# Kernel tuning notes

Hardware: AMD Instinct MI355X
Metric: run time of the kernel (lower is better)

## Reference

```python
import jax, jax.numpy as jnp
import numpy as np

D_MODEL = 1024
N_HEAD = 16
D_K = D_MODEL // N_HEAD


def setup_inputs() -> dict:
    key = jax.random.key(0)
    ks = jax.random.split(key, 11)
    B, S = 2, 2048
    std = 1.0 / np.sqrt(D_MODEL)
    inp = {
        "Q": jax.random.normal(ks[0], (B, S, D_MODEL), jnp.float32),
        "K": jax.random.normal(ks[1], (B, S, D_MODEL), jnp.float32),
        "V": jax.random.normal(ks[2], (B, S, D_MODEL), jnp.float32),
        "Wq": jax.random.normal(ks[3], (D_MODEL, D_MODEL), jnp.float32) * std,
        "bq": jnp.zeros((D_MODEL,), jnp.float32),
        "Wk": jax.random.normal(ks[4], (D_MODEL, D_MODEL), jnp.float32) * std,
        "bk": jnp.zeros((D_MODEL,), jnp.float32),
        "Wv": jax.random.normal(ks[5], (D_MODEL, D_MODEL), jnp.float32) * std,
        "bv": jnp.zeros((D_MODEL,), jnp.float32),
        "Wo": jax.random.normal(ks[6], (D_MODEL, D_MODEL), jnp.float32) * std,
        "bo": jnp.zeros((D_MODEL,), jnp.float32),
    }
    return inp


def _split_heads(x):
    # [B, S, D] -> [B, H, S, d_k]
    B, S, _ = x.shape
    return x.reshape(B, S, N_HEAD, D_K).transpose(0, 2, 1, 3)


def reference(Q, K, V, Wq, bq, Wk, bk, Wv, bv, Wo, bo):
    q = _split_heads(Q @ Wq.T + bq)   # [B,H,S,dk]
    k = _split_heads(K @ Wk.T + bk)
    v = _split_heads(V @ Wv.T + bv)
    scale = 1.0 / jnp.sqrt(jnp.float32(D_K))
    scores = jnp.einsum("bhqd,bhkd->bhqk", q, k) * scale
    attn = jax.nn.softmax(scores, axis=-1)
    ctx = jnp.einsum("bhqk,bhkd->bhqd", attn, v)  # [B,H,S,dk]
    B, H, S, dk = ctx.shape
    ctx = ctx.transpose(0, 2, 1, 3).reshape(B, S, H * dk)
    return ctx @ Wo.T + bo
```

## Files before the change

kernel.cpp:

```cpp
#include <hip/hip_runtime.h>
#include <hip/hip_bf16.h>
#include <cstdint>
#include <cstddef>
#include <cmath>

typedef __attribute__((ext_vector_type(8))) short short8;
typedef __attribute__((ext_vector_type(4))) short short4_t;
typedef __attribute__((ext_vector_type(4))) float f32x4;
typedef __attribute__((ext_vector_type(16))) float f32x16;

constexpr int B_ = 2, S_ = 2048, H_ = 16, DK_ = 64, DM_ = 1024;

__device__ inline unsigned short f2bf(float x) {
  union { float f; unsigned u; } c; c.f = x;
  unsigned r = c.u + 0x7FFF + ((c.u >> 16) & 1);
  return (unsigned short)(r >> 16);
}

__device__ inline float ex2(float x) {
#if __has_builtin(__builtin_amdgcn_exp2f)
  return __builtin_amdgcn_exp2f(x);
#else
  return exp2f(x);
#endif
}

__device__ inline unsigned pkbf(float lo, float hi) {
  unsigned u;
  asm("v_cvt_pk_bf16_f32 %0, %1, %2" : "=v"(u) : "v"(lo), "v"(hi));
  return u;
}

__device__ inline f32x4 mfma16(short8 a, short8 b, f32x4 c) {
  return __builtin_amdgcn_mfma_f32_16x16x32_bf16(a, b, c, 0, 0, 0);
}
__device__ inline f32x16 mfma32(short8 a, short8 b, f32x16 c) {
  return __builtin_amdgcn_mfma_f32_32x32x16_bf16(a, b, c, 0, 0, 0);
}

__device__ inline void glds16(const unsigned short* g, unsigned short* l) {
  __builtin_amdgcn_global_load_lds(
      (const __attribute__((address_space(1))) unsigned int*)g,
      (__attribute__((address_space(3))) unsigned int*)l, 16, 0, 0);
}

__global__ __launch_bounds__(256) void cvt_all(
    const float* __restrict__ Q, const float* __restrict__ K,
    const float* __restrict__ V, const float* __restrict__ Wq,
    const float* __restrict__ Wk, const float* __restrict__ Wv,
    const float* __restrict__ Wo, unsigned short* __restrict__ Qb,
    unsigned short* __restrict__ Kb, unsigned short* __restrict__ Vb,
    unsigned short* __restrict__ Wqb, unsigned short* __restrict__ Wkb,
    unsigned short* __restrict__ Wvb, unsigned short* __restrict__ Wob) {
  int bid = blockIdx.x;
  const float* in; unsigned short* out; int off;
  if (bid < 4096)       { in = Q;  out = Qb;  off = bid; }
  else if (bid < 8192)  { in = K;  out = Kb;  off = bid - 4096; }
  else if (bid < 12288) { in = V;  out = Vb;  off = bid - 8192; }
  else if (bid < 13312) { in = Wq; out = Wqb; off = bid - 12288; }
  else if (bid < 14336) { in = Wk; out = Wkb; off = bid - 13312; }
  else if (bid < 15360) { in = Wv; out = Wvb; off = bid - 14336; }
  else                  { in = Wo; out = Wob; off = bid - 15360; }
  int i = off * 256 + threadIdx.x;
  float4 f = ((const float4*)in)[i];
  uint2 o;
  o.x = pkbf(f.x, f.y);
  o.y = pkbf(f.z, f.w);
  ((uint2*)out)[i] = o;
}

__device__ inline void store_out(float* p, float v) { *p = v; }
__device__ inline void store_out(unsigned short* p, float v) { *p = f2bf(v); }

template <typename OUT_T>
__device__ inline void gemm_body(const unsigned short* __restrict__ A,
                                 const unsigned short* __restrict__ Bw,
                                 const float* __restrict__ bias,
                                 OUT_T* __restrict__ C, float cscale,
                                 int bm, int bn) {
  constexpr int Kd = 1024, Nd = 1024;
  __shared__ unsigned short As[128][64];
  __shared__ unsigned short Bs[64][64];

  const int tid = threadIdx.x;
  const int lane = tid & 63, wave = tid >> 6;
  const int li = lane & 15, lg = lane >> 4;
  const int wm = wave >> 1, wn = wave & 1;

  const f32x4 zero4 = {0.f, 0.f, 0.f, 0.f};
  f32x4 acc[4][2];
#pragma unroll
  for (int i = 0; i < 4; i++)
#pragma unroll
    for (int j = 0; j < 2; j++) acc[i][j] = zero4;

  const int stg_row = tid >> 3;
  const int stg_col = (tid & 7) * 8;
  const unsigned short* Ag = A + (size_t)(bm * 128 + stg_row) * Kd + stg_col;
  const unsigned short* Bg = Bw + (size_t)(bn * 64 + stg_row) * Kd + stg_col;

  for (int kt = 0; kt < Kd; kt += 64) {
#pragma unroll
    for (int i = 0; i < 4; i++)
      glds16(Ag + (size_t)(i * 32) * Kd + kt, &As[i * 32 + stg_row][stg_col]);
#pragma unroll
    for (int i = 0; i < 2; i++)
      glds16(Bg + (size_t)(i * 32) * Kd + kt, &Bs[i * 32 + stg_row][stg_col]);
    __syncthreads();

    short8 af[4][2], bf[2][2];
#pragma unroll
    for (int kb = 0; kb < 2; kb++) {
#pragma unroll
      for (int i = 0; i < 4; i++)
        af[i][kb] = *(const short8*)&As[wm * 64 + i * 16 + li][kb * 32 + lg * 8];
#pragma unroll
      for (int j = 0; j < 2; j++)
        bf[j][kb] = *(const short8*)&Bs[wn * 32 + j * 16 + li][kb * 32 + lg * 8];
    }
#pragma unroll
    for (int kb = 0; kb < 2; kb++)
#pragma unroll
      for (int i = 0; i < 4; i++)
#pragma unroll
        for (int j = 0; j < 2; j++)
          acc[i][j] = mfma16(af[i][kb], bf[j][kb], acc[i][j]);
    __syncthreads();
  }

#pragma unroll
  for (int j = 0; j < 2; j++) {
    int col = bn * 64 + wn * 32 + j * 16 + li;
    float bv = bias[col];
#pragma unroll
    for (int i = 0; i < 4; i++) {
      int row0 = bm * 128 + wm * 64 + i * 16 + lg * 4;
#pragma unroll
      for (int r = 0; r < 4; r++)
        store_out(&C[(size_t)(row0 + r) * Nd + col], (acc[i][j][r] + bv) * cscale);
    }
  }
}

__global__ __launch_bounds__(256) void gemm_qkv(
    const unsigned short* __restrict__ Aq, const unsigned short* __restrict__ Ak,
    const unsigned short* __restrict__ Av, const unsigned short* __restrict__ Bq,
    const unsigned short* __restrict__ Bk, const unsigned short* __restrict__ Bv,
    const float* __restrict__ bq, const float* __restrict__ bk,
    const float* __restrict__ bv, unsigned short* __restrict__ Cq,
    unsigned short* __restrict__ Ck, unsigned short* __restrict__ Cv,
    float qscale) {
  const int n = blockIdx.x;
  const int xcd = n & 7, m = n >> 3;
  const int z = m >> 6, idx = m & 63;
  const int bm = xcd * 4 + (idx >> 4), bn = idx & 15;
  const unsigned short* A = z == 0 ? Aq : z == 1 ? Ak : Av;
  const unsigned short* Bw = z == 0 ? Bq : z == 1 ? Bk : Bv;
  const float* bi = z == 0 ? bq : z == 1 ? bk : bv;
  unsigned short* C = z == 0 ? Cq : z == 1 ? Ck : Cv;
  gemm_body(A, Bw, bi, C, z == 0 ? qscale : 1.0f, bm, bn);
}

__global__ __launch_bounds__(256) void gemm_out(
    const unsigned short* __restrict__ A, const unsigned short* __restrict__ Bw,
    const float* __restrict__ bias, float* __restrict__ C) {
  const int n = blockIdx.x;
  const int xcd = n & 7, m = n >> 3;
  const int bm = xcd * 4 + (m >> 4), bn = m & 15;
  gemm_body(A, Bw, bias, C, 1.0f, bm, bn);
}

struct V4 { short8 v[4]; };

__device__ __forceinline__ void attn_tile_step(
    int kt, int buf, int NT,
    const unsigned short* kg, const unsigned short* vg,
    unsigned short* KsAll, unsigned short* VtAll,
    int srow, int sc, int scs, int key2, int dq,
    const short8* qf, int l31, int h,
    V4& vc, V4& vn, f32x16* po, float& m_i, float& l_i) {
  unsigned short* KsB = KsAll + buf * (128 * 64);
  unsigned short* VtB = VtAll + buf * (64 * 128);
  unsigned short* KsO = KsAll + (buf ^ 1) * (128 * 64);

  asm volatile("s_waitcnt vmcnt(0)" ::: "memory");
  __builtin_amdgcn_sched_barrier(0);

#pragma unroll
  for (int j = 0; j < 16; j++) {
    const int half = j >> 3, jj = j & 7;
    unsigned w = (unsigned)(unsigned short)vc.v[half][jj] |
                 ((unsigned)(unsigned short)vc.v[2 + half][jj] << 16);
    const int slot = (key2 >> 3) ^ j;
    *(unsigned*)&VtB[(dq * 16 + j) * 128 + slot * 8 + (key2 & 7)] = w;
  }

  if (kt + 1 < NT) {
    const unsigned short* vp =
        vg + (size_t)((kt + 1) * 128 + key2) * DM_ + dq * 16;
    vn.v[0] = *(const short8*)(vp);
    vn.v[1] = *(const short8*)(vp + 8);
    vn.v[2] = *(const short8*)(vp + DM_);
    vn.v[3] = *(const short8*)(vp + DM_ + 8);
  }

  asm volatile("s_waitcnt lgkmcnt(0)" ::: "memory");
  __builtin_amdgcn_sched_barrier(0);
  __builtin_amdgcn_s_barrier();
  __builtin_amdgcn_sched_barrier(0);

  if (kt + 1 < NT) {
    const unsigned short* kgt = kg + (size_t)((kt + 1) * 128) * DM_;
#pragma unroll
    for (int i = 0; i < 4; i++)
      glds16(kgt + (size_t)(i * 32 + srow) * DM_ + scs,
             &KsO[(i * 32 + srow) * 64 + sc * 8]);
  }
  __builtin_amdgcn_sched_barrier(0);

  f32x16 sacc[4];
#pragma unroll
  for (int kb = 0; kb < 4; kb++)
#pragma unroll
    for (int r = 0; r < 16; r++) sacc[kb][r] = 0.f;

  __builtin_amdgcn_s_setprio(1);
#pragma unroll
  for (int tq = 0; tq < 4; tq++) {
    const int sl = ((((tq << 1) | h) ^ (l31 & 7))) * 8;
#pragma unroll
    for (int kb = 0; kb < 4; kb++) {
      short8 kf = *(const short8*)&KsB[(kb * 32 + l31) * 64 + sl];
      sacc[kb] = mfma32(kf, qf[tq], sacc[kb]);
    }
  }
  __builtin_amdgcn_s_setprio(0);

  float mx = -1e30f;
#pragma unroll
  for (int kb = 0; kb < 4; kb++)
#pragma unroll
    for (int r = 0; r < 16; r += 4)
      mx = fmaxf(mx, fmaxf(fmaxf(sacc[kb][r], sacc[kb][r + 1]),
                           fmaxf(sacc[kb][r + 2], sacc[kb][r + 3])));
  mx = fmaxf(mx, __shfl_xor(mx, 32));

  if (!__all(mx - m_i <= 8.0f)) {
    float mn = fmaxf(m_i, mx);
    float al = ex2(m_i - mn);
    m_i = mn;
    l_i *= al;
#pragma unroll
    for (int db = 0; db < 2; db++)
#pragma unroll
      for (int r = 0; r < 16; r++) po[db][r] *= al;
  }

  float s0 = 0.f, s1 = 0.f, s2 = 0.f, s3 = 0.f;
#pragma unroll
  for (int kb = 0; kb < 4; kb++) {
#pragma unroll
    for (int r = 0; r < 16; r += 4) {
      float p0 = ex2(sacc[kb][r] - m_i);
      float p1 = ex2(sacc[kb][r + 1] - m_i);
      float p2 = ex2(sacc[kb][r + 2] - m_i);
      float p3 = ex2(sacc[kb][r + 3] - m_i);
      sacc[kb][r] = p0; sacc[kb][r + 1] = p1;
      sacc[kb][r + 2] = p2; sacc[kb][r + 3] = p3;
      s0 += p0; s1 += p1; s2 += p2; s3 += p3;
    }
    unsigned u[4][2];
#pragma unroll
    for (int qd = 0; qd < 4; qd++) {
      u[qd][0] = pkbf(sacc[kb][4 * qd], sacc[kb][4 * qd + 1]);
      u[qd][1] = pkbf(sacc[kb][4 * qd + 2], sacc[kb][4 * qd + 3]);
    }
#pragma unroll
    for (int tt = 0; tt < 2; tt++) {
      const int tp = 2 * kb + tt, qe = tt * 2;
      unsigned X0 = u[qe][0], X1 = u[qe][1];
      unsigned Y0 = u[qe + 1][0], Y1 = u[qe + 1][1];
      unsigned sX0 = __shfl_xor(X0, 32), sX1 = __shfl_xor(X1, 32);
      unsigned sY0 = __shfl_xor(Y0, 32), sY1 = __shfl_xor(Y1, 32);
      union { unsigned w[4]; short8 v8; } fr;
      fr.w[0] = h ? sY0 : X0;
      fr.w[1] = h ? sY1 : X1;
      fr.w[2] = h ? Y0 : sX0;
      fr.w[3] = h ? Y1 : sX1;
      const int slbase = (tp << 1) | h;
#pragma unroll
      for (int db = 0; db < 2; db++) {
        const int row = db * 32 + l31;
        short8 vf = *(const short8*)
            &VtB[row * 128 + (slbase ^ (l31 & 15)) * 8];
        po[db] = mfma32(vf, fr.v8, po[db]);
      }
    }
  }
  float sum = (s0 + s1) + (s2 + s3);
  sum += __shfl_xor(sum, 32);
  l_i += sum;
}

__global__ __launch_bounds__(256, 2) void attn_fwd(
    const unsigned short* __restrict__ q, const unsigned short* __restrict__ k,
    const unsigned short* __restrict__ v, unsigned short* __restrict__ ctx) {
  __shared__ unsigned short Ks[2][128][64];
  __shared__ unsigned short Vt[2][64][128];

  const int tid = threadIdx.x;
  const int lane = tid & 63, wave = tid >> 6;
  const int l31 = lane & 31, h = lane >> 5;
  const int n = blockIdx.x;
  const int xcd = n & 7, m = n >> 3;
  const int bh = xcd * 4 + (m & 3);
  const int qt = m >> 2;
  const int b = bh >> 4, hd = bh & 15;

  const int qrow = qt * 128 + wave * 32 + l31;
  const unsigned short* qg = q + (size_t)(b * S_ + qrow) * DM_ + hd * DK_;
  short8 qf[4];
#pragma unroll
  for (int t = 0; t < 4; t++) qf[t] = *(const short8*)(qg + t * 16 + h * 8);

  f32x16 po[2];
#pragma unroll
  for (int db = 0; db < 2; db++)
#pragma unroll
    for (int r = 0; r < 16; r++) po[db][r] = 0.f;
  float m_i = -1e30f, l_i = 0.f;

  const int srow = tid >> 3, sc = tid & 7;
  const int scs = (sc ^ (srow & 7)) * 8;
  const unsigned short* kg = k + (size_t)(b * S_) * DM_ + hd * DK_;

  const int key2 = (tid & 63) * 2, dq = tid >> 6;
  const unsigned short* vg = v + (size_t)(b * S_) * DM_ + hd * DK_;

  const int NT = S_ / 128;

#pragma unroll
  for (int i = 0; i < 4; i++)
    glds16(kg + (size_t)(i * 32 + srow) * DM_ + scs,
           &Ks[0][i * 32 + srow][sc * 8]);
  V4 va, vb;
  {
    const unsigned short* vp = vg + (size_t)key2 * DM_ + dq * 16;
    va.v[0] = *(const short8*)(vp);
    va.v[1] = *(const short8*)(vp + 8);
    va.v[2] = *(const short8*)(vp + DM_);
    va.v[3] = *(const short8*)(vp + DM_ + 8);
  }

  unsigned short* KsAll = &Ks[0][0][0];
  unsigned short* VtAll = &Vt[0][0][0];
  for (int it = 0; it < NT; it += 2) {
    attn_tile_step(it, 0, NT, kg, vg, KsAll, VtAll, srow, sc, scs, key2, dq,
                   qf, l31, h, va, vb, po, m_i, l_i);
    attn_tile_step(it + 1, 1, NT, kg, vg, KsAll, VtAll, srow, sc, scs, key2,
                   dq, qf, l31, h, vb, va, po, m_i, l_i);
  }

  float rl = 1.0f / l_i;
  unsigned short* cg = ctx + (size_t)(b * S_ + qrow) * DM_ + hd * DK_;
#pragma unroll
  for (int db = 0; db < 2; db++)
#pragma unroll
    for (int rq = 0; rq < 4; rq++) {
      uint2 w2;
      w2.x = pkbf(po[db][4 * rq] * rl, po[db][4 * rq + 1] * rl);
      w2.y = pkbf(po[db][4 * rq + 2] * rl, po[db][4 * rq + 3] * rl);
      *(uint2*)(cg + db * 32 + 8 * rq + 4 * h) = w2;
    }
}

extern "C" void kernel_launch(void* const* d_in, const int* in_sizes, int n_in,
                              void* d_out, int out_size, void* d_ws, size_t ws_size,
                              hipStream_t stream) {
  const float* Q  = (const float*)d_in[0];
  const float* Kx = (const float*)d_in[1];
  const float* V  = (const float*)d_in[2];
  const float* Wq = (const float*)d_in[3];
  const float* bq = (const float*)d_in[4];
  const float* Wk = (const float*)d_in[5];
  const float* bk = (const float*)d_in[6];
  const float* Wv = (const float*)d_in[7];
  const float* bv = (const float*)d_in[8];
  const float* Wo = (const float*)d_in[9];
  const float* bo = (const float*)d_in[10];
  float* out = (float*)d_out;

  char* ws = (char*)d_ws;
  const size_t MB = 1ull << 20;
  unsigned short* Qb  = (unsigned short*)(ws + 0 * MB);
  unsigned short* Kb  = (unsigned short*)(ws + 8 * MB);
  unsigned short* Vb  = (unsigned short*)(ws + 16 * MB);
  unsigned short* Wqb = (unsigned short*)(ws + 24 * MB);
  unsigned short* Wkb = (unsigned short*)(ws + 26 * MB);
  unsigned short* Wvb = (unsigned short*)(ws + 28 * MB);
  unsigned short* Wob = (unsigned short*)(ws + 30 * MB);
  unsigned short* qp  = (unsigned short*)(ws + 32 * MB);
  unsigned short* kp  = (unsigned short*)(ws + 40 * MB);
  unsigned short* vp  = (unsigned short*)(ws + 48 * MB);
  unsigned short* cx  = (unsigned short*)(ws + 56 * MB);

  cvt_all<<<16384, 256, 0, stream>>>(Q, Kx, V, Wq, Wk, Wv, Wo,
                                     Qb, Kb, Vb, Wqb, Wkb, Wvb, Wob);

  gemm_qkv<<<1536, 256, 0, stream>>>(
      Qb, Kb, Vb, Wqb, Wkb, Wvb, bq, bk, bv, qp, kp, vp, 0.18033688f);

  attn_fwd<<<512, 256, 0, stream>>>(qp, kp, vp, cx);

  gemm_out<<<512, 256, 0, stream>>>(cx, Wob, bo, out);
}
```

Before: 138.1 us.

## Double-buffer GEMM LDS tiles and raise wave priority around attention PV MFMAs

The projection GEMM body now uses two LDS buffers for A and B and prefetches the next K-tile with direct global-to-LDS loads while the current tile is consumed. This overlaps memory latency with MFMA work and drops one barrier per iteration. LDS use per block doubles, and the GEMM kernels are given a launch bound hinting three blocks per CU. The attention kernel also raises wave priority around the PV MFMA section to favor matrix issue over other waves.

```diff
diff --git a/kernel.cpp b/kernel.cpp
--- a/kernel.cpp
+++ b/kernel.cpp
@@ -78,9 +78,9 @@
                                  const float* __restrict__ bias,
                                  OUT_T* __restrict__ C, float cscale,
                                  int bm, int bn) {
-  constexpr int Kd = 1024, Nd = 1024;
-  __shared__ unsigned short As[128][64];
-  __shared__ unsigned short Bs[64][64];
+  constexpr int Kd = 1024, Nd = 1024, NSTEP = Kd / 64;
+  __shared__ unsigned short As[2][128][64];
+  __shared__ unsigned short Bs[2][64][64];
 
   const int tid = threadIdx.x;
   const int lane = tid & 63, wave = tid >> 6;
@@ -99,24 +99,44 @@
   const unsigned short* Ag = A + (size_t)(bm * 128 + stg_row) * Kd + stg_col;
   const unsigned short* Bg = Bw + (size_t)(bn * 64 + stg_row) * Kd + stg_col;
 
-  for (int kt = 0; kt < Kd; kt += 64) {
-#pragma unroll
-    for (int i = 0; i < 4; i++)
-      glds16(Ag + (size_t)(i * 32) * Kd + kt, &As[i * 32 + stg_row][stg_col]);
-#pragma unroll
-    for (int i = 0; i < 2; i++)
-      glds16(Bg + (size_t)(i * 32) * Kd + kt, &Bs[i * 32 + stg_row][stg_col]);
-    __syncthreads();
+#pragma unroll
+  for (int i = 0; i < 4; i++)
+    glds16(Ag + (size_t)(i * 32) * Kd, &As[0][i * 32 + stg_row][stg_col]);
+#pragma unroll
+  for (int i = 0; i < 2; i++)
+    glds16(Bg + (size_t)(i * 32) * Kd, &Bs[0][i * 32 + stg_row][stg_col]);
+
+  for (int kt = 0; kt < NSTEP; kt++) {
+    const int buf = kt & 1;
+    asm volatile("s_waitcnt vmcnt(0)" ::: "memory");
+    __builtin_amdgcn_sched_barrier(0);
+    __builtin_amdgcn_s_barrier();
+    __builtin_amdgcn_sched_barrier(0);
+
+    if (kt + 1 < NSTEP) {
+      const int kof = (kt + 1) * 64;
+#pragma unroll
+      for (int i = 0; i < 4; i++)
+        glds16(Ag + (size_t)(i * 32) * Kd + kof,
+               &As[buf ^ 1][i * 32 + stg_row][stg_col]);
+#pragma unroll
+      for (int i = 0; i < 2; i++)
+        glds16(Bg + (size_t)(i * 32) * Kd + kof,
+               &Bs[buf ^ 1][i * 32 + stg_row][stg_col]);
+    }
+    __builtin_amdgcn_sched_barrier(0);
 
     short8 af[4][2], bf[2][2];
 #pragma unroll
     for (int kb = 0; kb < 2; kb++) {
 #pragma unroll
       for (int i = 0; i < 4; i++)
-        af[i][kb] = *(const short8*)&As[wm * 64 + i * 16 + li][kb * 32 + lg * 8];
+        af[i][kb] =
+            *(const short8*)&As[buf][wm * 64 + i * 16 + li][kb * 32 + lg * 8];
 #pragma unroll
       for (int j = 0; j < 2; j++)
-        bf[j][kb] = *(const short8*)&Bs[wn * 32 + j * 16 + li][kb * 32 + lg * 8];
+        bf[j][kb] =
+            *(const short8*)&Bs[buf][wn * 32 + j * 16 + li][kb * 32 + lg * 8];
     }
 #pragma unroll
     for (int kb = 0; kb < 2; kb++)
@@ -125,7 +145,6 @@
 #pragma unroll
         for (int j = 0; j < 2; j++)
           acc[i][j] = mfma16(af[i][kb], bf[j][kb], acc[i][j]);
-    __syncthreads();
   }
 
 #pragma unroll
@@ -142,7 +161,7 @@
   }
 }
 
-__global__ __launch_bounds__(256) void gemm_qkv(
+__global__ __launch_bounds__(256, 3) void gemm_qkv(
     const unsigned short* __restrict__ Aq, const unsigned short* __restrict__ Ak,
     const unsigned short* __restrict__ Av, const unsigned short* __restrict__ Bq,
     const unsigned short* __restrict__ Bk, const unsigned short* __restrict__ Bv,
@@ -161,7 +180,7 @@
   gemm_body(A, Bw, bi, C, z == 0 ? qscale : 1.0f, bm, bn);
 }
 
-__global__ __launch_bounds__(256) void gemm_out(
+__global__ __launch_bounds__(256, 3) void gemm_out(
     const unsigned short* __restrict__ A, const unsigned short* __restrict__ Bw,
     const float* __restrict__ bias, float* __restrict__ C) {
   const int n = blockIdx.x;
@@ -275,6 +294,7 @@
       u[qd][0] = pkbf(sacc[kb][4 * qd], sacc[kb][4 * qd + 1]);
       u[qd][1] = pkbf(sacc[kb][4 * qd + 2], sacc[kb][4 * qd + 3]);
     }
+    __builtin_amdgcn_s_setprio(1);
 #pragma unroll
     for (int tt = 0; tt < 2; tt++) {
       const int tp = 2 * kb + tt, qe = tt * 2;
@@ -296,6 +316,7 @@
         po[db] = mfma32(vf, fr.v8, po[db]);
       }
     }
+    __builtin_amdgcn_s_setprio(0);
   }
   float sum = (s0 + s1) + (s2 + s3);
   sum += __shfl_xor(sum, 32);
```

After: 138.5 us. Within noise of the previous version (+0.3%).
